# Kernel optimization log

Measured on AMD Instinct MI355X. Metric: run time of the kernel, lower is better.

The kernel has to match this reference:

```python
import jax, jax.numpy as jnp
import numpy as np

# Winograd F(2x2, 3x3) transform matrices (standard Lavin & Gray form).
# The original torch module encodes B^T / A^T but applies them with elementwise
# mul (a bug that crashes); the intended math is Y = A^T [ (G g G^T) .* (B^T d B) ] A
# per 4x4 input tile with stride 2, which equals a valid 3x3 conv. We implement
# that intended Winograd computation faithfully and vectorized.
_BT = jnp.array([[1., 0., -1., 0.],
                 [0., 1., 1., 0.],
                 [0., -1., 1., 0.],
                 [0., 1., 0., -1.]], dtype=jnp.float32)
_G = jnp.array([[1., 0., 0.],
                [0.5, 0.5, 0.5],
                [0.5, -0.5, 0.5],
                [0., 0., 1.]], dtype=jnp.float32)
_AT = jnp.array([[1., 1., 1., 0.],
                 [0., 1., -1., -1.]], dtype=jnp.float32)


def setup_inputs() -> dict:
    key = jax.random.key(0)
    k1, k2 = jax.random.split(key)
    X = jax.random.normal(k1, (16, 32, 258, 258), dtype=jnp.float32)
    K = jax.random.normal(k2, (32, 32, 3, 3), dtype=jnp.float32)
    return {"X": X, "K": K}


def _winograd_conv(X, K):
    B_, C, H, W = X.shape
    Fo = K.shape[0]
    blocks = (H - 3) // 2 + 1  # number of 2x2 output tiles per spatial dim

    # Kernel transform: U = G K G^T  -> (Fo, C, 4, 4)
    U = jnp.einsum('ij,fcjk,lk->fcil', _G, K, _G)

    # Extract overlapping 4x4 tiles with stride 2: (B, C, blocks, blocks, 4, 4)
    i0 = jnp.arange(blocks) * 2
    win = i0[:, None] + jnp.arange(4)[None, :]          # (blocks, 4)
    tiles = X[:, :, win, :]                              # (B, C, blocks, 4, W)
    tiles = tiles[:, :, :, :, win]                       # (B, C, blocks, 4, blocks, 4)
    tiles = tiles.transpose(0, 1, 2, 4, 3, 5)            # (B, C, p, q, 4, 4)

    # Input transform: V = B^T d B
    V = jnp.einsum('ij,bcpqjk,lk->bcpqil', _BT, tiles, _BT)

    # Elementwise multiply in transform domain, summed over input channels
    M = jnp.einsum('fcil,bcpqil->bfpqil', U, V)          # (B, Fo, p, q, 4, 4)

    # Inverse transform: Y = A^T M A -> (B, Fo, p, q, 2, 2)
    Y = jnp.einsum('ij,bfpqjk,lk->bfpqil', _AT, M, _AT)

    # Stitch 2x2 tiles back: (B, Fo, 2*blocks, 2*blocks)
    out = Y.transpose(0, 1, 2, 4, 3, 5).reshape(B_, Fo, 2 * blocks, 2 * blocks)
    return out


def reference(X, K):
    return _winograd_conv(X, K)
```

## Files before the change

### kernel.cpp

```cpp
#include <hip/hip_runtime.h>
#include <stdint.h>

typedef __attribute__((ext_vector_type(8))) short bf16x8;
typedef __attribute__((ext_vector_type(4))) float f32x4;
typedef __attribute__((ext_vector_type(2))) float f32x2;

__device__ inline float bflo(uint32_t w) { union { uint32_t i; float f; } v; v.i = w << 16; return v.f; }
__device__ inline float bfhi(uint32_t w) { union { uint32_t i; float f; } v; v.i = w & 0xffff0000u; return v.f; }
__device__ inline uint32_t f2bf(float f) { union { float f; uint32_t i; } v; v.f = f; return (v.i + 0x8000u) >> 16; }
__device__ inline uint32_t pk(float lo, float hi) { return f2bf(lo) | (f2bf(hi) << 16); }

__device__ inline f32x2 pka(f32x2 a, f32x2 b) {
    f32x2 d; asm("v_pk_add_f32 %0, %1, %2" : "=v"(d) : "v"(a), "v"(b)); return d;
}
__device__ inline f32x2 pks(f32x2 a, f32x2 b) {
    f32x2 d; asm("v_pk_add_f32 %0, %1, %2 neg_lo:[0,1] neg_hi:[0,1]" : "=v"(d) : "v"(a), "v"(b)); return d;
}
__device__ inline uint32_t cvtpk2(float lo, float hi) {
    uint32_t r; asm("v_cvt_pk_bf16_f32 %0, %1, %2" : "=v"(r) : "v"(lo), "v"(hi)); return r;
}
__device__ inline uint32_t cvtpk(f32x2 v) { return cvtpk2(v.x, v.y); }
__device__ inline f32x2 unpk(uint32_t w) {
    union { uint32_t u; float f; } lo, hi; lo.u = w << 16; hi.u = w & 0xffff0000u;
    return (f32x2){lo.f, hi.f};
}

__global__ __launch_bounds__(256) void wg_filter(const float* __restrict__ Kk, uint32_t* __restrict__ Ud)
{
    const int idx = blockIdx.x * 256 + threadIdx.x;
    if (idx >= 512) return;
    const int cp = idx & 15, f = idx >> 4;
    float u[2][16];
    #pragma unroll
    for (int h = 0; h < 2; h++) {
        const float* kp = Kk + (f * 32 + cp * 2 + h) * 9;
        float k00 = kp[0], k01 = kp[1], k02 = kp[2];
        float k10 = kp[3], k11 = kp[4], k12 = kp[5];
        float k20 = kp[6], k21 = kp[7], k22 = kp[8];
        float t[4][3];
        t[0][0] = k00; t[0][1] = k01; t[0][2] = k02;
        t[1][0] = 0.5f * (k00 + k10 + k20); t[1][1] = 0.5f * (k01 + k11 + k21); t[1][2] = 0.5f * (k02 + k12 + k22);
        t[2][0] = 0.5f * (k00 - k10 + k20); t[2][1] = 0.5f * (k01 - k11 + k21); t[2][2] = 0.5f * (k02 - k12 + k22);
        t[3][0] = k20; t[3][1] = k21; t[3][2] = k22;
        #pragma unroll
        for (int i = 0; i < 4; i++) {
            float a0 = t[i][0], a1 = t[i][1], a2 = t[i][2];
            u[h][i * 4 + 0] = a0;
            u[h][i * 4 + 1] = 0.5f * (a0 + a1 + a2);
            u[h][i * 4 + 2] = 0.5f * (a0 - a1 + a2);
            u[h][i * 4 + 3] = a2;
        }
    }
    const int base = ((cp >> 2) * 32 + f) * 4 + (cp & 3);
    #pragma unroll
    for (int p = 0; p < 16; p++) Ud[p * 512 + base] = pk(u[0][p], u[1][p]);
}

__global__ __launch_bounds__(256, 4) void wg_main(
    const float* __restrict__ X, const uint16_t* __restrict__ U, float* __restrict__ out)
{
    __shared__ __align__(16) uint32_t Pl[2912];

    const int tid = threadIdx.x;
    const int lin  = blockIdx.x + 16 * (blockIdx.y + 32 * blockIdx.z);
    const int work = (lin & 7) * 1024 + (lin >> 3);
    const int qb = work & 15;
    const int pb = (work >> 4) & 31;
    const int b  = work >> 9;
    const int y0 = pb * 8, x0 = qb * 16;

    for (int s = tid; s < 1440; s += 256) {
        const int pr = s / 90;
        const int r  = s - pr * 90;
        const int row = r / 9, seg = r - row * 9;
        const float* g0 = X + ((size_t)((b * 32 + pr * 2) * 258 + y0 + row)) * 258 + x0 + seg * 2;
        float2 a = *(const float2*)g0;
        float2 c = *(const float2*)(g0 + 258 * 258);
        uint2 w;
        w.x = cvtpk2(a.x, c.x);
        w.y = cvtpk2(a.y, c.y);
        *(uint2*)&Pl[pr * 182 + row * 18 + seg * 2] = w;
    }
    __syncthreads();

    const int wave = tid >> 6, lane = tid & 63;
    const int fh = wave & 1, tb = wave >> 1;
    const int l15 = lane & 15, lq = lane >> 4;
    const uint16_t* Ub = U + (lq * 32 + fh * 16 + l15) * 8;

    const int tt = tb * 16 + l15;
    const int trr = tt >> 3, tcc = tt & 7;
    const uint32_t* pbase = Pl + (lq * 4) * 182 + (trr * 2) * 18 + tcc * 2;

    float y[4][4];
    #pragma unroll
    for (int r = 0; r < 4; r++)
        #pragma unroll
        for (int j = 0; j < 4; j++) y[r][j] = 0.f;

    #pragma unroll
    for (int i = 0; i < 4; i++) {
        const int ra = (i == 0) ? 0 : (i == 2) ? 2 : 1;
        const int rb = (i == 3) ? 3 : (i == 2) ? 1 : 2;

        bf16x8 a_reg[4];
        #pragma unroll
        for (int l = 0; l < 4; l++)
            a_reg[l] = *(const bf16x8*)(Ub + (i * 4 + l) * 1024);

        uint32_t va[4][4];
        #pragma unroll
        for (int pp = 0; pp < 4; pp++) {
            const uint32_t* pr_ = pbase + pp * 182;
            uint2 wa0 = *(const uint2*)(pr_ + ra * 18);
            uint2 wa1 = *(const uint2*)(pr_ + ra * 18 + 2);
            uint2 wb0 = *(const uint2*)(pr_ + rb * 18);
            uint2 wb1 = *(const uint2*)(pr_ + rb * 18 + 2);
            f32x2 da0 = unpk(wa0.x), da1 = unpk(wa0.y), da2 = unpk(wa1.x), da3 = unpk(wa1.y);
            f32x2 db0 = unpk(wb0.x), db1 = unpk(wb0.y), db2 = unpk(wb1.x), db3 = unpk(wb1.y);
            f32x2 e0, e1, e2, e3;
            if (i == 1) {
                e0 = pka(da0, db0); e1 = pka(da1, db1); e2 = pka(da2, db2); e3 = pka(da3, db3);
            } else {
                e0 = pks(da0, db0); e1 = pks(da1, db1); e2 = pks(da2, db2); e3 = pks(da3, db3);
            }
            va[0][pp] = cvtpk(pks(e0, e2));
            va[1][pp] = cvtpk(pka(e1, e2));
            va[2][pp] = cvtpk(pks(e2, e1));
            va[3][pp] = cvtpk(pks(e1, e3));
        }

        f32x4 acc[4];
        #pragma unroll
        for (int l = 0; l < 4; l++) {
            union { uint32_t u[4]; bf16x8 v; } cvt;
            cvt.u[0] = va[l][0]; cvt.u[1] = va[l][1];
            cvt.u[2] = va[l][2]; cvt.u[3] = va[l][3];
            acc[l] = __builtin_amdgcn_mfma_f32_16x16x32_bf16(a_reg[l], cvt.v,
                        (f32x4){0.f, 0.f, 0.f, 0.f}, 0, 0, 0);
        }

        #pragma unroll
        for (int r = 0; r < 4; r++) {
            float m0 = acc[0][r], m1 = acc[1][r], m2 = acc[2][r], m3 = acc[3][r];
            float c0 = m0 + m1 + m2, c1 = m1 - m2 - m3;
            if (i == 0)      { y[r][0] += c0; y[r][1] += c1; }
            else if (i == 1) { y[r][0] += c0; y[r][1] += c1; y[r][2] += c0; y[r][3] += c1; }
            else if (i == 2) { y[r][0] += c0; y[r][1] += c1; y[r][2] -= c0; y[r][3] -= c1; }
            else             { y[r][2] -= c0; y[r][3] -= c1; }
        }
    }

    const int p = pb * 4 + trr, q = qb * 8 + tcc;
    #pragma unroll
    for (int r = 0; r < 4; r++) {
        const int f = fh * 16 + lq * 4 + r;
        float* op = out + ((size_t)(b * 32 + f) * 256 + 2 * p) * 256 + 2 * q;
        *(float2*)op = make_float2(y[r][0], y[r][1]);
        *(float2*)(op + 256) = make_float2(y[r][2], y[r][3]);
    }
}

__device__ inline uint16_t f2bf16_rne(float f) {
    union { float f; uint32_t i; } v; v.f = f;
    uint32_t x = v.i;
    uint32_t r = x + 0x7fffu + ((x >> 16) & 1u);
    return (uint16_t)(r >> 16);
}
__global__ __launch_bounds__(256) void winograd_fallback(
    const float* __restrict__ X, const float* __restrict__ K, float* __restrict__ out)
{
    __shared__ uint16_t Ul[16384];
    __shared__ uint16_t Vl[16384];
    __shared__ uint16_t Pl[32 * 242];
    const int tid = threadIdx.x;
    const int qb = blockIdx.x, pb = blockIdx.y, b = blockIdx.z;
    for (int idx = tid; idx < 1024; idx += 256) {
        const int f = idx >> 5, c = idx & 31;
        const float* kp = K + (f * 32 + c) * 9;
        float k00 = kp[0], k01 = kp[1], k02 = kp[2];
        float k10 = kp[3], k11 = kp[4], k12 = kp[5];
        float k20 = kp[6], k21 = kp[7], k22 = kp[8];
        float t[4][3];
        t[0][0] = k00; t[0][1] = k01; t[0][2] = k02;
        t[1][0] = 0.5f * (k00 + k10 + k20); t[1][1] = 0.5f * (k01 + k11 + k21); t[1][2] = 0.5f * (k02 + k12 + k22);
        t[2][0] = 0.5f * (k00 - k10 + k20); t[2][1] = 0.5f * (k01 - k11 + k21); t[2][2] = 0.5f * (k02 - k12 + k22);
        t[3][0] = k20; t[3][1] = k21; t[3][2] = k22;
        const int ubase = ((c >> 3) * 32 + f) * 8 + (c & 7);
        #pragma unroll
        for (int i = 0; i < 4; i++) {
            float a0 = t[i][0], a1 = t[i][1], a2 = t[i][2];
            Ul[(i * 4 + 0) * 1024 + ubase] = f2bf16_rne(a0);
            Ul[(i * 4 + 1) * 1024 + ubase] = f2bf16_rne(0.5f * (a0 + a1 + a2));
            Ul[(i * 4 + 2) * 1024 + ubase] = f2bf16_rne(0.5f * (a0 - a1 + a2));
            Ul[(i * 4 + 3) * 1024 + ubase] = f2bf16_rne(a2);
        }
    }
    const int y0 = pb * 8, x0 = qb * 16;
    for (int s = tid; s < 2880; s += 256) {
        const int c = s / 90;
        const int r = s % 90;
        const int row = r / 9, seg = r % 9;
        const float* gp = X + ((b * 32 + c) * 258 + (y0 + row)) * 258 + x0 + seg * 2;
        float2 g = *(const float2*)gp;
        uint32_t packed = (uint32_t)f2bf16_rne(g.x) | ((uint32_t)f2bf16_rne(g.y) << 16);
        *(uint32_t*)&Pl[c * 242 + row * 24 + seg * 2] = packed;
    }
    __syncthreads();
    for (int idx = tid; idx < 1024; idx += 256) {
        const int c = idx & 31, tt = idx >> 5;
        const int tr = tt >> 3, tc = tt & 7;
        const uint16_t* pp = &Pl[c * 242 + (tr * 2) * 24 + tc * 2];
        float d[4][4];
        #pragma unroll
        for (int j = 0; j < 4; j++) {
            uint32_t w0 = *(const uint32_t*)&pp[j * 24];
            uint32_t w1 = *(const uint32_t*)&pp[j * 24 + 2];
            d[j][0] = bflo(w0); d[j][1] = bfhi(w0);
            d[j][2] = bflo(w1); d[j][3] = bfhi(w1);
        }
        float bt[4][4];
        #pragma unroll
        for (int k = 0; k < 4; k++) {
            bt[0][k] = d[0][k] - d[2][k];
            bt[1][k] = d[1][k] + d[2][k];
            bt[2][k] = d[2][k] - d[1][k];
            bt[3][k] = d[1][k] - d[3][k];
        }
        const int vbase = (((tt >> 4) * 4 + (c >> 3)) * 16 + (tt & 15)) * 8 + (c & 7);
        #pragma unroll
        for (int i = 0; i < 4; i++) {
            float b0 = bt[i][0], b1 = bt[i][1], b2 = bt[i][2], b3 = bt[i][3];
            Vl[(i * 4 + 0) * 1024 + vbase] = f2bf16_rne(b0 - b2);
            Vl[(i * 4 + 1) * 1024 + vbase] = f2bf16_rne(b1 + b2);
            Vl[(i * 4 + 2) * 1024 + vbase] = f2bf16_rne(b2 - b1);
            Vl[(i * 4 + 3) * 1024 + vbase] = f2bf16_rne(b1 - b3);
        }
    }
    __syncthreads();
    const int wave = tid >> 6, lane = tid & 63;
    const int fh = wave & 1, tb = wave >> 1;
    const int l15 = lane & 15, lq = lane >> 4;
    f32x4 acc[16];
    #pragma unroll
    for (int p = 0; p < 16; p++) acc[p] = (f32x4){0.f, 0.f, 0.f, 0.f};
    #pragma unroll
    for (int p = 0; p < 16; p++) {
        bf16x8 a = *(const bf16x8*)&Ul[p * 1024 + (lq * 32 + fh * 16 + l15) * 8];
        bf16x8 bv = *(const bf16x8*)&Vl[p * 1024 + ((tb * 4 + lq) * 16 + l15) * 8];
        acc[p] = __builtin_amdgcn_mfma_f32_16x16x32_bf16(a, bv, acc[p], 0, 0, 0);
    }
    #pragma unroll
    for (int r = 0; r < 4; r++) {
        const int f = fh * 16 + lq * 4 + r;
        const int t = tb * 16 + l15;
        const int tr = t >> 3, tc = t & 7;
        const int p = pb * 4 + tr, q = qb * 8 + tc;
        float m[4][4];
        #pragma unroll
        for (int i = 0; i < 4; i++)
            #pragma unroll
            for (int l = 0; l < 4; l++)
                m[i][l] = acc[i * 4 + l][r];
        float s0[4], s1[4];
        #pragma unroll
        for (int k = 0; k < 4; k++) {
            s0[k] = m[0][k] + m[1][k] + m[2][k];
            s1[k] = m[1][k] - m[2][k] - m[3][k];
        }
        float* op = out + ((size_t)(b * 32 + f) * 256 + 2 * p) * 256 + 2 * q;
        *(float2*)op = make_float2(s0[0] + s0[1] + s0[2], s0[1] - s0[2] - s0[3]);
        *(float2*)(op + 256) = make_float2(s1[0] + s1[1] + s1[2], s1[1] - s1[2] - s1[3]);
    }
}

extern "C" void kernel_launch(void* const* d_in, const int* in_sizes, int n_in,
                              void* d_out, int out_size, void* d_ws, size_t ws_size,
                              hipStream_t stream) {
    const float* X = (const float*)d_in[0];
    const float* K = (const float*)d_in[1];
    float* out = (float*)d_out;
    dim3 grid(16, 32, 16);
    if (ws_size >= 32768) {
        wg_filter<<<2, 256, 0, stream>>>(K, (uint32_t*)d_ws);
        wg_main<<<grid, 256, 0, stream>>>(X, (const uint16_t*)d_ws, out);
    } else {
        winograd_fallback<<<grid, 256, 0, stream>>>(X, K, out);
    }
}
```

Measured before the change: 94.31 us.

## Make wg_main persistent over four tiles with double-buffered LDS prefetch

Each block now handles four consecutive tiles instead of one, and the grid shrinks to 2048 blocks. The next tile's input is loaded into registers while the current tile computes, then written to a second LDS buffer, so global-load latency overlaps with MFMA work. In exchange the block uses twice the LDS, the launch bound drops to 3 blocks per CU, and register pressure rises. The block-to-work swizzle also changes.

```diff
diff --git a/kernel.cpp b/kernel.cpp
--- a/kernel.cpp
+++ b/kernel.cpp
@@ -56,108 +56,184 @@
     for (int p = 0; p < 16; p++) Ud[p * 512 + base] = pk(u[0][p], u[1][p]);
 }
 
-__global__ __launch_bounds__(256, 4) void wg_main(
+template<int I>
+__device__ __forceinline__ void wg_chunk(const uint32_t* __restrict__ pbase,
+                                         const uint16_t* __restrict__ Ub,
+                                         float (&y)[4][4])
+{
+    const int ra = (I == 0) ? 0 : (I == 2) ? 2 : 1;
+    const int rb = (I == 3) ? 3 : (I == 2) ? 1 : 2;
+
+    bf16x8 a_reg[4];
+    #pragma unroll
+    for (int l = 0; l < 4; l++)
+        a_reg[l] = *(const bf16x8*)(Ub + (I * 4 + l) * 1024);
+
+    uint32_t va[4][4];
+    #pragma unroll
+    for (int pp = 0; pp < 4; pp++) {
+        const uint32_t* pr_ = pbase + pp * 182;
+        uint2 wa0 = *(const uint2*)(pr_ + ra * 18);
+        uint2 wa1 = *(const uint2*)(pr_ + ra * 18 + 2);
+        uint2 wb0 = *(const uint2*)(pr_ + rb * 18);
+        uint2 wb1 = *(const uint2*)(pr_ + rb * 18 + 2);
+        f32x2 da0 = unpk(wa0.x), da1 = unpk(wa0.y), da2 = unpk(wa1.x), da3 = unpk(wa1.y);
+        f32x2 db0 = unpk(wb0.x), db1 = unpk(wb0.y), db2 = unpk(wb1.x), db3 = unpk(wb1.y);
+        f32x2 e0, e1, e2, e3;
+        if (I == 1) {
+            e0 = pka(da0, db0); e1 = pka(da1, db1); e2 = pka(da2, db2); e3 = pka(da3, db3);
+        } else {
+            e0 = pks(da0, db0); e1 = pks(da1, db1); e2 = pks(da2, db2); e3 = pks(da3, db3);
+        }
+        va[0][pp] = cvtpk(pks(e0, e2));
+        va[1][pp] = cvtpk(pka(e1, e2));
+        va[2][pp] = cvtpk(pks(e2, e1));
+        va[3][pp] = cvtpk(pks(e1, e3));
+    }
+
+    f32x4 acc[4];
+    #pragma unroll
+    for (int l = 0; l < 4; l++) {
+        union { uint32_t u[4]; bf16x8 v; } cvt;
+        cvt.u[0] = va[l][0]; cvt.u[1] = va[l][1];
+        cvt.u[2] = va[l][2]; cvt.u[3] = va[l][3];
+        acc[l] = __builtin_amdgcn_mfma_f32_16x16x32_bf16(a_reg[l], cvt.v,
+                    (f32x4){0.f, 0.f, 0.f, 0.f}, 0, 0, 0);
+    }
+
+    #pragma unroll
+    for (int r = 0; r < 4; r++) {
+        float m0 = acc[0][r], m1 = acc[1][r], m2 = acc[2][r], m3 = acc[3][r];
+        float c0 = m0 + m1 + m2, c1 = m1 - m2 - m3;
+        if (I == 0)      { y[r][0] += c0; y[r][1] += c1; }
+        else if (I == 1) { y[r][0] += c0; y[r][1] += c1; y[r][2] += c0; y[r][3] += c1; }
+        else if (I == 2) { y[r][0] += c0; y[r][1] += c1; y[r][2] -= c0; y[r][3] -= c1; }
+        else             { y[r][2] -= c0; y[r][3] -= c1; }
+    }
+}
+
+__global__ __launch_bounds__(256, 3) void wg_main(
     const float* __restrict__ X, const uint16_t* __restrict__ U, float* __restrict__ out)
 {
-    __shared__ __align__(16) uint32_t Pl[2912];
+    __shared__ __align__(16) uint32_t Pl[2][2912];
 
     const int tid = threadIdx.x;
-    const int lin  = blockIdx.x + 16 * (blockIdx.y + 32 * blockIdx.z);
-    const int work = (lin & 7) * 1024 + (lin >> 3);
-    const int qb = work & 15;
-    const int pb = (work >> 4) & 31;
-    const int b  = work >> 9;
-    const int y0 = pb * 8, x0 = qb * 16;
-
-    for (int s = tid; s < 1440; s += 256) {
-        const int pr = s / 90;
-        const int r  = s - pr * 90;
-        const int row = r / 9, seg = r - row * 9;
-        const float* g0 = X + ((size_t)((b * 32 + pr * 2) * 258 + y0 + row)) * 258 + x0 + seg * 2;
-        float2 a = *(const float2*)g0;
-        float2 c = *(const float2*)(g0 + 258 * 258);
-        uint2 w;
-        w.x = cvtpk2(a.x, c.x);
-        w.y = cvtpk2(a.y, c.y);
-        *(uint2*)&Pl[pr * 182 + row * 18 + seg * 2] = w;
-    }
-    __syncthreads();
+    const int swz = (blockIdx.x & 7) * 256 + (blockIdx.x >> 3);
+    const int wbase = swz * 4;
 
     const int wave = tid >> 6, lane = tid & 63;
     const int fh = wave & 1, tb = wave >> 1;
     const int l15 = lane & 15, lq = lane >> 4;
     const uint16_t* Ub = U + (lq * 32 + fh * 16 + l15) * 8;
-
     const int tt = tb * 16 + l15;
     const int trr = tt >> 3, tcc = tt & 7;
-    const uint32_t* pbase = Pl + (lq * 4) * 182 + (trr * 2) * 18 + tcc * 2;
-
-    float y[4][4];
-    #pragma unroll
-    for (int r = 0; r < 4; r++)
-        #pragma unroll
-        for (int j = 0; j < 4; j++) y[r][j] = 0.f;
-
-    #pragma unroll
-    for (int i = 0; i < 4; i++) {
-        const int ra = (i == 0) ? 0 : (i == 2) ? 2 : 1;
-        const int rb = (i == 3) ? 3 : (i == 2) ? 1 : 2;
-
-        bf16x8 a_reg[4];
-        #pragma unroll
-        for (int l = 0; l < 4; l++)
-            a_reg[l] = *(const bf16x8*)(Ub + (i * 4 + l) * 1024);
-
-        uint32_t va[4][4];
-        #pragma unroll
-        for (int pp = 0; pp < 4; pp++) {
-            const uint32_t* pr_ = pbase + pp * 182;
-            uint2 wa0 = *(const uint2*)(pr_ + ra * 18);
-            uint2 wa1 = *(const uint2*)(pr_ + ra * 18 + 2);
-            uint2 wb0 = *(const uint2*)(pr_ + rb * 18);
-            uint2 wb1 = *(const uint2*)(pr_ + rb * 18 + 2);
-            f32x2 da0 = unpk(wa0.x), da1 = unpk(wa0.y), da2 = unpk(wa1.x), da3 = unpk(wa1.y);
-            f32x2 db0 = unpk(wb0.x), db1 = unpk(wb0.y), db2 = unpk(wb1.x), db3 = unpk(wb1.y);
-            f32x2 e0, e1, e2, e3;
-            if (i == 1) {
-                e0 = pka(da0, db0); e1 = pka(da1, db1); e2 = pka(da2, db2); e3 = pka(da3, db3);
-            } else {
-                e0 = pks(da0, db0); e1 = pks(da1, db1); e2 = pks(da2, db2); e3 = pks(da3, db3);
-            }
-            va[0][pp] = cvtpk(pks(e0, e2));
-            va[1][pp] = cvtpk(pka(e1, e2));
-            va[2][pp] = cvtpk(pks(e2, e1));
-            va[3][pp] = cvtpk(pks(e1, e3));
-        }
-
-        f32x4 acc[4];
-        #pragma unroll
-        for (int l = 0; l < 4; l++) {
-            union { uint32_t u[4]; bf16x8 v; } cvt;
-            cvt.u[0] = va[l][0]; cvt.u[1] = va[l][1];
-            cvt.u[2] = va[l][2]; cvt.u[3] = va[l][3];
-            acc[l] = __builtin_amdgcn_mfma_f32_16x16x32_bf16(a_reg[l], cvt.v,
-                        (f32x4){0.f, 0.f, 0.f, 0.f}, 0, 0, 0);
-        }
-
-        #pragma unroll
-        for (int r = 0; r < 4; r++) {
-            float m0 = acc[0][r], m1 = acc[1][r], m2 = acc[2][r], m3 = acc[3][r];
-            float c0 = m0 + m1 + m2, c1 = m1 - m2 - m3;
-            if (i == 0)      { y[r][0] += c0; y[r][1] += c1; }
-            else if (i == 1) { y[r][0] += c0; y[r][1] += c1; y[r][2] += c0; y[r][3] += c1; }
-            else if (i == 2) { y[r][0] += c0; y[r][1] += c1; y[r][2] -= c0; y[r][3] -= c1; }
-            else             { y[r][2] -= c0; y[r][3] -= c1; }
-        }
-    }
-
-    const int p = pb * 4 + trr, q = qb * 8 + tcc;
-    #pragma unroll
-    for (int r = 0; r < 4; r++) {
-        const int f = fh * 16 + lq * 4 + r;
-        float* op = out + ((size_t)(b * 32 + f) * 256 + 2 * p) * 256 + 2 * q;
-        *(float2*)op = make_float2(y[r][0], y[r][1]);
-        *(float2*)(op + 256) = make_float2(y[r][2], y[r][3]);
+    const int lofs = (lq * 4) * 182 + (trr * 2) * 18 + tcc * 2;
+
+    float2 Ar[3], Cr[3];
+
+    {
+        const int w0 = wbase;
+        const int qb = w0 & 15, pb = (w0 >> 4) & 31, bb = w0 >> 9;
+        #pragma unroll
+        for (int half = 0; half < 2; half++) {
+            #pragma unroll
+            for (int t = 0; t < 3; t++) {
+                const int s = tid + (half * 3 + t) * 256;
+                if (s < 1440) {
+                    const int pr = s / 90, r = s - pr * 90, row = r / 9, seg = r - row * 9;
+                    const float* g0 = X + ((size_t)((bb * 32 + pr * 2) * 258 + pb * 8 + row)) * 258 + qb * 16 + seg * 2;
+                    Ar[t] = *(const float2*)g0;
+                    Cr[t] = *(const float2*)(g0 + 66564);
+                }
+            }
+            #pragma unroll
+            for (int t = 0; t < 3; t++) {
+                const int s = tid + (half * 3 + t) * 256;
+                if (s < 1440) {
+                    const int pr = s / 90, r = s - pr * 90, row = r / 9, seg = r - row * 9;
+                    uint2 w; w.x = cvtpk2(Ar[t].x, Cr[t].x); w.y = cvtpk2(Ar[t].y, Cr[t].y);
+                    *(uint2*)&Pl[0][pr * 182 + row * 18 + seg * 2] = w;
+                }
+            }
+        }
+    }
+    __syncthreads();
+
+    #pragma unroll
+    for (int k = 0; k < 4; ++k) {
+        const int work = wbase + k;
+        const int qb = work & 15, pb = (work >> 4) & 31, bb = work >> 9;
+        const int wn = work + 1;
+        const int qn = wn & 15, pn = (wn >> 4) & 31, bn = wn >> 9;
+        const int nbuf = (k + 1) & 1;
+
+        if (k < 3) {
+            #pragma unroll
+            for (int t = 0; t < 3; t++) {
+                const int s = tid + t * 256;
+                const int pr = s / 90, r = s - pr * 90, row = r / 9, seg = r - row * 9;
+                const float* g0 = X + ((size_t)((bn * 32 + pr * 2) * 258 + pn * 8 + row)) * 258 + qn * 16 + seg * 2;
+                Ar[t] = *(const float2*)g0;
+                Cr[t] = *(const float2*)(g0 + 66564);
+            }
+        }
+
+        const uint32_t* pbase = &Pl[k & 1][lofs];
+        float y[4][4];
+        #pragma unroll
+        for (int r = 0; r < 4; r++)
+            #pragma unroll
+            for (int j = 0; j < 4; j++) y[r][j] = 0.f;
+
+        wg_chunk<0>(pbase, Ub, y);
+        wg_chunk<1>(pbase, Ub, y);
+
+        if (k < 3) {
+            #pragma unroll
+            for (int t = 0; t < 3; t++) {
+                const int s = tid + t * 256;
+                const int pr = s / 90, r = s - pr * 90, row = r / 9, seg = r - row * 9;
+                uint2 w; w.x = cvtpk2(Ar[t].x, Cr[t].x); w.y = cvtpk2(Ar[t].y, Cr[t].y);
+                *(uint2*)&Pl[nbuf][pr * 182 + row * 18 + seg * 2] = w;
+            }
+            #pragma unroll
+            for (int t = 0; t < 3; t++) {
+                const int s = tid + (3 + t) * 256;
+                if (s < 1440) {
+                    const int pr = s / 90, r = s - pr * 90, row = r / 9, seg = r - row * 9;
+                    const float* g0 = X + ((size_t)((bn * 32 + pr * 2) * 258 + pn * 8 + row)) * 258 + qn * 16 + seg * 2;
+                    Ar[t] = *(const float2*)g0;
+                    Cr[t] = *(const float2*)(g0 + 66564);
+                }
+            }
+        }
+
+        wg_chunk<2>(pbase, Ub, y);
+        wg_chunk<3>(pbase, Ub, y);
+
+        {
+            const int p = pb * 4 + trr, q = qb * 8 + tcc;
+            #pragma unroll
+            for (int r = 0; r < 4; r++) {
+                const int f = fh * 16 + lq * 4 + r;
+                float* op = out + ((size_t)(bb * 32 + f) * 256 + 2 * p) * 256 + 2 * q;
+                *(float2*)op = make_float2(y[r][0], y[r][1]);
+                *(float2*)(op + 256) = make_float2(y[r][2], y[r][3]);
+            }
+        }
+
+        if (k < 3) {
+            #pragma unroll
+            for (int t = 0; t < 3; t++) {
+                const int s = tid + (3 + t) * 256;
+                if (s < 1440) {
+                    const int pr = s / 90, r = s - pr * 90, row = r / 9, seg = r - row * 9;
+                    uint2 w; w.x = cvtpk2(Ar[t].x, Cr[t].x); w.y = cvtpk2(Ar[t].y, Cr[t].y);
+                    *(uint2*)&Pl[nbuf][pr * 182 + row * 18 + seg * 2] = w;
+                }
+            }
+        }
+        __syncthreads();
     }
 }
 
@@ -280,11 +356,11 @@
     const float* X = (const float*)d_in[0];
     const float* K = (const float*)d_in[1];
     float* out = (float*)d_out;
-    dim3 grid(16, 32, 16);
     if (ws_size >= 32768) {
         wg_filter<<<2, 256, 0, stream>>>(K, (uint32_t*)d_ws);
-        wg_main<<<grid, 256, 0, stream>>>(X, (const uint16_t*)d_ws, out);
+        wg_main<<<2048, 256, 0, stream>>>(X, (const uint16_t*)d_ws, out);
     } else {
+        dim3 grid(16, 32, 16);
         winograd_fallback<<<grid, 256, 0, stream>>>(X, K, out);
     }
 }
```

Result: slower. 97.27 us (+3.1%).
